# Kernel tuning notes

Hardware: AMD Instinct MI355X
Metric: run time of the kernel (lower is better)

## Reference

```python
import jax, jax.numpy as jnp
import numpy as np

B, D_IN, E, H, V = 4096, 4096, 2048, 2048, 32000


def setup_inputs() -> dict:
    key = jax.random.key(0)
    ks = jax.random.split(key, 24)
    s = 0.02
    p = lambda k, shape: (jax.random.normal(k, shape, dtype=jnp.float32) * s)
    return {
        "input": jax.random.normal(ks[0], (B, D_IN), dtype=jnp.float32),
        "hidden": jnp.zeros((B, H), dtype=jnp.float32),
        "cell": jnp.zeros((B, H), dtype=jnp.float32),
        # embedding linear (input_size -> emb_size), stored as [in, out]
        "We": p(ks[1], (D_IN, E)), "be": p(ks[2], (E,)),
        # x-to-gate linears (emb -> hidden)
        "Wf": p(ks[3], (E, H)), "bf": p(ks[4], (H,)),
        "Wi": p(ks[5], (E, H)), "bi": p(ks[6], (H,)),
        "Wc": p(ks[7], (E, H)), "bc": p(ks[8], (H,)),
        "Wo": p(ks[9], (E, H)), "bo": p(ks[10], (H,)),
        # hidden-to-gate linears (hidden -> hidden)
        "Uf": p(ks[11], (H, H)), "bhf": p(ks[12], (H,)),
        "Ui": p(ks[13], (H, H)), "bhi": p(ks[14], (H,)),
        "Uc": p(ks[15], (H, H)), "bhc": p(ks[16], (H,)),
        "Uo": p(ks[17], (H, H)), "bho": p(ks[18], (H,)),
        # output head (hidden -> output_size)
        "Wend": p(ks[19], (H, V)), "bend": p(ks[20], (V,)),
    }


def reference(input, hidden, cell,
              We, be, Wf, bf, Wi, bi, Wc, bc, Wo, bo,
              Uf, bhf, Ui, bhi, Uc, bhc, Uo, bho, Wend, bend):
    # embedded = Linear(input)
    emb = input @ We + be                                  # [B, E]
    f = jax.nn.sigmoid(emb @ Wf + bf + hidden @ Uf + bhf)  # forget gate [B, H]
    i = jax.nn.sigmoid(emb @ Wi + bi + hidden @ Ui + bhi)  # input gate
    g = jnp.tanh(emb @ Wc + bc + hidden @ Uc + bhc)        # candidate cell
    new_cell = f * cell + i * g
    o = jax.nn.sigmoid(emb @ Wo + bo + hidden @ Uo + bho)  # output gate
    new_hidden = o * jnp.tanh(new_cell)
    out = jax.nn.log_softmax(new_hidden @ Wend + bend, axis=1)  # [B, V]
    return (out, new_hidden, new_cell)
```

## Files before the change

kernel.cpp:

```cpp
#include <hip/hip_runtime.h>
#include <stdint.h>

#define B_DIM 4096
#define DIN   4096
#define E_DIM 2048
#define H_DIM 2048
#define V_DIM 32000

typedef __attribute__((ext_vector_type(8))) short s8v;
typedef __attribute__((ext_vector_type(4))) float f4v;
typedef __attribute__((ext_vector_type(4))) int   i4v;
typedef __attribute__((ext_vector_type(8))) int   i8v;
typedef __attribute__((ext_vector_type(4))) uint  u4v;
typedef __attribute__((ext_vector_type(4))) float f4n;

__device__ __forceinline__ ushort f2bf(float f) {
    union { float f; uint32_t u; } v; v.f = f;
    uint32_t u = v.u;
    return (ushort)((u + 0x7FFFu + ((u >> 16) & 1u)) >> 16);
}
__device__ __forceinline__ float bf2f(ushort h) {
    union { uint32_t u; float f; } v; v.u = ((uint32_t)h) << 16;
    return v.f;
}

__device__ __forceinline__ uint8_t f2fp8(float x) {
    union { float f; uint32_t u; } v; v.f = x;
    uint8_t sign = (uint8_t)((v.u >> 24) & 0x80u);
    uint32_t a = v.u & 0x7FFFFFFFu;
    if (a >= 0x43E00000u) return sign | 0x7E;
    uint32_t r = a + 0x0007FFFFu + ((a >> 20) & 1u);
    int e = (int)(r >> 23) - 127 + 7;
    if (e <= 0) {
        float s = fabsf(x);
        int q = (int)(s * 512.0f + 0.5f);
        if (q > 7) q = 7;
        return sign | (uint8_t)q;
    }
    uint32_t m = (r >> 20) & 7u;
    uint8_t b = (uint8_t)((e << 3) | m);
    if (b == 0x7F) b = 0x7E;
    return sign | b;
}

__global__ void k_cvt(const float* __restrict__ src, ushort* __restrict__ dst, int n4) {
    int i = blockIdx.x * blockDim.x + threadIdx.x;
    if (i >= n4) return;
    float4 v = *(const float4*)(src + (size_t)i * 4);
    ushort4 o;
    o.x = f2bf(v.x); o.y = f2bf(v.y); o.z = f2bf(v.z); o.w = f2bf(v.w);
    *(ushort4*)(dst + (size_t)i * 4) = o;
}

__global__ void k_cvt_hidden(const float* __restrict__ src, ushort* __restrict__ dst) {
    int i = blockIdx.x * blockDim.x + threadIdx.x;
    int b = i >> 9;
    int c = (i & 511) << 2;
    float4 v = *(const float4*)(src + (size_t)b * H_DIM + c);
    ushort4 o;
    o.x = f2bf(v.x); o.y = f2bf(v.y); o.z = f2bf(v.z); o.w = f2bf(v.w);
    *(ushort4*)(dst + (size_t)b * 4096 + 2048 + c) = o;
}

__global__ void k_transpose_bf16(const float* __restrict__ src, ushort* __restrict__ dst,
                                 int srcCols, int dstStride, int dstRowOff, int dstColOff) {
    __shared__ float tile[32][33];
    int tx = threadIdx.x, ty = threadIdx.y;
    int n0 = blockIdx.x * 32, k0 = blockIdx.y * 32;
#pragma unroll
    for (int i = 0; i < 4; i++)
        tile[ty + 8 * i][tx] = src[(size_t)(k0 + ty + 8 * i) * srcCols + n0 + tx];
    __syncthreads();
#pragma unroll
    for (int i = 0; i < 4; i++) {
        int n = ty + 8 * i;
        dst[(size_t)(dstRowOff + n0 + n) * dstStride + dstColOff + k0 + tx] = f2bf(tile[tx][n]);
    }
}

__global__ void k_transpose_fp8(const float* __restrict__ src, uint8_t* __restrict__ dst,
                                int srcCols, int dstStride) {
    __shared__ float tile[32][33];
    int tx = threadIdx.x, ty = threadIdx.y;
    int n0 = blockIdx.x * 32, k0 = blockIdx.y * 32;
#pragma unroll
    for (int i = 0; i < 4; i++)
        tile[ty + 8 * i][tx] = src[(size_t)(k0 + ty + 8 * i) * srcCols + n0 + tx];
    __syncthreads();
#pragma unroll
    for (int i = 0; i < 4; i++) {
        int n = ty + 8 * i;
        dst[(size_t)(n0 + n) * dstStride + k0 + tx] = f2fp8(tile[tx][n] * 32.0f);
    }
}

__global__ void k_transpose_gate8(const float* __restrict__ W0, const float* __restrict__ W1,
                                  const float* __restrict__ W2, const float* __restrict__ W3,
                                  const float* __restrict__ U0, const float* __restrict__ U1,
                                  const float* __restrict__ U2, const float* __restrict__ U3,
                                  ushort* __restrict__ dst) {
    const float* srcs[8] = {W0, W1, W2, W3, U0, U1, U2, U3};
    int z = blockIdx.z;
    const float* src = srcs[z];
    int g = z & 3;
    int dstColOff = (z >> 2) << 11;
    __shared__ float tile[32][33];
    int tx = threadIdx.x, ty = threadIdx.y;
    int n0 = blockIdx.x * 32, k0 = blockIdx.y * 32;
#pragma unroll
    for (int i = 0; i < 4; i++)
        tile[ty + 8 * i][tx] = src[(size_t)(k0 + ty + 8 * i) * H_DIM + n0 + tx];
    __syncthreads();
#pragma unroll
    for (int i = 0; i < 4; i++) {
        int h = n0 + ty + 8 * i;
        int drow = ((h >> 5) << 7) + (((h >> 4) & 1) << 6) + (g << 4) + (h & 15);
        dst[(size_t)drow * 4096 + dstColOff + k0 + tx] = f2bf(tile[tx][ty + 8 * i]);
    }
}

__global__ void k_biaspack(const float* __restrict__ b0, const float* __restrict__ bh0,
                           const float* __restrict__ b1, const float* __restrict__ bh1,
                           const float* __restrict__ b2, const float* __restrict__ bh2,
                           const float* __restrict__ b3, const float* __restrict__ bh3,
                           float* __restrict__ out) {
    int h = blockIdx.x * blockDim.x + threadIdx.x;
    if (h >= H_DIM) return;
    int base = ((h >> 5) << 7) + (((h >> 4) & 1) << 6) + (h & 15);
    out[base]      = b0[h] + bh0[h];
    out[base + 16] = b1[h] + bh1[h];
    out[base + 32] = b2[h] + bh2[h];
    out[base + 48] = b3[h] + bh3[h];
}

template<int EPI>
__global__ __launch_bounds__(256, 2)
void k_gemm_bt(const ushort* __restrict__ A, const ushort* __restrict__ Bt,
               void* __restrict__ Cv, const float* __restrict__ bias,
               int M, int N, int K, int lda, int ldb, int ldc,
               const float* __restrict__ cell, float* __restrict__ outH,
               float* __restrict__ outC, uint8_t* __restrict__ hidF8) {
    __shared__ __align__(16) ushort ldsA[128 * 64];
    __shared__ __align__(16) ushort ldsB[128 * 64];
    const int t = threadIdx.x;
    const int wid = t >> 6, lane = t & 63;

    int bid = blockIdx.x;
    int mt  = ((bid & 7) << 2) | ((bid >> 3) & 3);
    int nt  = bid >> 5;
    int m0  = mt << 7, n0 = nt << 7;

    f4v acc[4][4];
#pragma unroll
    for (int i = 0; i < 4; i++)
#pragma unroll
        for (int j = 0; j < 4; j++) acc[i][j] = (f4v){0.f, 0.f, 0.f, 0.f};

    const int wr = wid >> 1, wc = wid & 1;

    const int kTiles = K >> 6;
    for (int kt = 0; kt < kTiles; ++kt) {
#pragma unroll
        for (int c = 0; c < 4; ++c) {
            int idx = c * 256 + wid * 64 + lane;
            int row = idx >> 3;
            int kb  = (idx & 7) << 4;
            const ushort* gA = A  + (size_t)(m0 + row) * lda + (kt << 6) + (kb >> 1);
            const ushort* gB = Bt + (size_t)(n0 + row) * ldb + (kt << 6) + (kb >> 1);
            char* lA = (char*)ldsA + (size_t)(c * 256 + wid * 64) * 16;
            char* lB = (char*)ldsB + (size_t)(c * 256 + wid * 64) * 16;
            __builtin_amdgcn_global_load_lds((const __attribute__((address_space(1))) void*)gA,
                                             (__attribute__((address_space(3))) void*)lA, 16, 0, 0);
            __builtin_amdgcn_global_load_lds((const __attribute__((address_space(1))) void*)gB,
                                             (__attribute__((address_space(3))) void*)lB, 16, 0, 0);
        }
        __syncthreads();

#pragma unroll
        for (int ks = 0; ks < 2; ++ks) {
            s8v af[4], bfr[4];
#pragma unroll
            for (int m = 0; m < 4; ++m) {
                int r = wr * 64 + m * 16 + (lane & 15);
                int kb = ks * 64 + ((lane >> 4) << 4);
                af[m] = *(const s8v*)((const char*)ldsA + r * 128 + kb);
            }
#pragma unroll
            for (int n = 0; n < 4; ++n) {
                int r = wc * 64 + n * 16 + (lane & 15);
                int kb = ks * 64 + ((lane >> 4) << 4);
                bfr[n] = *(const s8v*)((const char*)ldsB + r * 128 + kb);
            }
#pragma unroll
            for (int m = 0; m < 4; ++m)
#pragma unroll
                for (int n = 0; n < 4; ++n)
                    acc[m][n] = __builtin_amdgcn_mfma_f32_16x16x32_bf16(af[m], bfr[n], acc[m][n], 0, 0, 0);
        }
        __syncthreads();
    }

    if (EPI == 1) {
#pragma unroll
        for (int n = 0; n < 4; ++n) {
            int cg = n0 + wc * 64 + n * 16 + (lane & 15);
            float bv = bias[cg];
#pragma unroll
            for (int m = 0; m < 4; ++m) {
                int rbase = m0 + wr * 64 + m * 16 + ((lane >> 4) << 2);
#pragma unroll
                for (int r = 0; r < 4; ++r)
                    ((ushort*)Cv)[(size_t)(rbase + r) * ldc + cg] = f2bf(acc[m][n][r] + bv);
            }
        }
    } else {
        int h = (n0 >> 2) + wc * 16 + (lane & 15);
        float bv[4];
#pragma unroll
        for (int n = 0; n < 4; ++n) bv[n] = bias[n0 + wc * 64 + n * 16 + (lane & 15)];
#pragma unroll
        for (int m = 0; m < 4; ++m) {
            int rbase = m0 + wr * 64 + m * 16 + ((lane >> 4) << 2);
#pragma unroll
            for (int r = 0; r < 4; ++r) {
                int b = rbase + r;
                float pf_ = acc[m][0][r] + bv[0];
                float pi_ = acc[m][1][r] + bv[1];
                float pc_ = acc[m][2][r] + bv[2];
                float po_ = acc[m][3][r] + bv[3];
                float fg = 1.f / (1.f + __expf(-pf_));
                float ig = 1.f / (1.f + __expf(-pi_));
                float gg = tanhf(pc_);
                float og = 1.f / (1.f + __expf(-po_));
                size_t off = (size_t)b * H_DIM + h;
                float nc = fg * cell[off] + ig * gg;
                float nh = og * tanhf(nc);
                outC[off] = nc;
                outH[off] = nh;
                hidF8[off] = f2fp8(nh * 8.0f);
            }
        }
    }
}

__global__ __launch_bounds__(256, 3)
void k_gemm_mx(const uint8_t* __restrict__ A, const uint8_t* __restrict__ Bt,
               ushort* __restrict__ Lbf, const float* __restrict__ bias,
               float2* __restrict__ partials, int N, int K, int ldc, int ncb) {
    __shared__ __align__(16) uint8_t ldsAB[2][128 * 128];
    __shared__ float2 smStat[256];
    const int t = threadIdx.x;
    const int wid = t >> 6, lane = t & 63;
    const int wrr = wid >> 1, wcc = wid & 1;

    int bid = blockIdx.x;
    int mt  = ((bid & 7) << 2) | ((bid >> 3) & 3);
    int nt  = bid >> 5;
    int m0  = mt << 7, n0 = nt << 7;

    int offA[4], offB[4];
#pragma unroll
    for (int c = 0; c < 4; ++c) {
        int idx = c * 256 + t;
        int row = idx >> 3;
        int cb  = ((idx & 7) ^ (row & 7)) << 4;
        offA[c] = (m0 + row) * K + cb;
        offB[c] = (n0 + row) * K + cb;
    }

    f4v acc[4][4];
#pragma unroll
    for (int i = 0; i < 4; ++i)
#pragma unroll
        for (int j = 0; j < 4; ++j) acc[i][j] = (f4v){0.f, 0.f, 0.f, 0.f};

    const int l15 = lane & 15;
    const int sw  = (lane & 7) << 4;
    const int o0  = ((lane >> 4) << 5) ^ sw;
    const int o1  = o0 ^ 16;

    const int kTiles = K >> 7;
    for (int kt = 0; kt < kTiles; ++kt) {
#pragma unroll
        for (int c = 0; c < 4; ++c) {
            __builtin_amdgcn_global_load_lds(
                (const __attribute__((address_space(1))) void*)(A + offA[c] + (kt << 7)),
                (__attribute__((address_space(3))) void*)&ldsAB[0][(c * 256 + wid * 64) * 16], 16, 0, 0);
            __builtin_amdgcn_global_load_lds(
                (const __attribute__((address_space(1))) void*)(Bt + offB[c] + (kt << 7)),
                (__attribute__((address_space(3))) void*)&ldsAB[1][(c * 256 + wid * 64) * 16], 16, 0, 0);
        }
        __syncthreads();

        i8v af[4], bf[4];
#pragma unroll
        for (int m = 0; m < 4; ++m) {
            int row = wrr * 64 + m * 16 + l15;
            i4v lo = *(const i4v*)&ldsAB[0][row * 128 + o0];
            i4v hi = *(const i4v*)&ldsAB[0][row * 128 + o1];
            af[m] = __builtin_shufflevector(lo, hi, 0, 1, 2, 3, 4, 5, 6, 7);
        }
#pragma unroll
        for (int n = 0; n < 4; ++n) {
            int row = wcc * 64 + n * 16 + l15;
            i4v lo = *(const i4v*)&ldsAB[1][row * 128 + o0];
            i4v hi = *(const i4v*)&ldsAB[1][row * 128 + o1];
            bf[n] = __builtin_shufflevector(lo, hi, 0, 1, 2, 3, 4, 5, 6, 7);
        }
#pragma unroll
        for (int m = 0; m < 4; ++m)
#pragma unroll
            for (int n = 0; n < 4; ++n)
                acc[m][n] = __builtin_amdgcn_mfma_scale_f32_16x16x128_f8f6f4(
                    af[m], bf[n], acc[m][n], 0, 0, 0, 124, 0, 122);
        __syncthreads();
    }

    float bv[4];
#pragma unroll
    for (int n = 0; n < 4; ++n) bv[n] = bias[n0 + wcc * 64 + n * 16 + l15];
    ushort* ctile = (ushort*)&ldsAB[0][0];
#pragma unroll
    for (int m = 0; m < 4; ++m) {
#pragma unroll
        for (int r = 0; r < 4; ++r) {
            int rl = wrr * 64 + m * 16 + ((lane >> 4) << 2) + r;
            float v[4];
#pragma unroll
            for (int n = 0; n < 4; ++n) {
                v[n] = acc[m][n][r] + bv[n];
                ctile[rl * 128 + wcc * 64 + n * 16 + l15] = f2bf(v[n]);
            }
            float mx = fmaxf(fmaxf(v[0], v[1]), fmaxf(v[2], v[3]));
            float ss = __expf(v[0] - mx) + __expf(v[1] - mx) +
                       __expf(v[2] - mx) + __expf(v[3] - mx);
#pragma unroll
            for (int off = 1; off < 16; off <<= 1) {
                float mo = __shfl_xor(mx, off);
                float so = __shfl_xor(ss, off);
                float nm = fmaxf(mx, mo);
                ss = ss * __expf(mx - nm) + so * __expf(mo - nm);
                mx = nm;
            }
            if (l15 == 0) smStat[wcc * 128 + rl] = make_float2(mx, ss);
        }
    }
    __syncthreads();
    if (t < 128) {
        float2 a = smStat[t], b = smStat[128 + t];
        float M = fmaxf(a.x, b.x);
        float S = a.y * __expf(a.x - M) + b.y * __expf(b.x - M);
        partials[(size_t)(m0 + t) * ncb + nt] = make_float2(M, S);
    }
#pragma unroll
    for (int i = 0; i < 8; ++i) {
        int idx = i * 256 + t;
        int row = idx >> 4;
        int c16 = idx & 15;
        u4v val = *(const u4v*)&ctile[row * 128 + c16 * 8];
        __builtin_nontemporal_store(val, (u4v*)&Lbf[(size_t)(m0 + row) * ldc + n0 + c16 * 8]);
    }
}

__global__ void k_lsefin(const float2* __restrict__ part, float* __restrict__ lse, int ncb) {
    int row = blockIdx.x;
    int l = threadIdx.x;
    float M = -1e30f, S = 0.f;
    for (int i = l; i < ncb; i += 64) {
        float2 p = part[(size_t)row * ncb + i];
        float nm = fmaxf(M, p.x);
        S = S * __expf(M - nm) + p.y * __expf(p.x - nm);
        M = nm;
    }
#pragma unroll
    for (int off = 1; off < 64; off <<= 1) {
        float Mo = __shfl_xor(M, off);
        float So = __shfl_xor(S, off);
        float nm = fmaxf(M, Mo);
        S = S * __expf(M - nm) + So * __expf(Mo - nm);
        M = nm;
    }
    if (l == 0) lse[row] = M + logf(S);
}

__global__ void k_norm(const ushort* __restrict__ Lbf, const float* __restrict__ lse,
                       float* __restrict__ out) {
    int b = blockIdx.y;
    int c8 = blockIdx.x * blockDim.x + threadIdx.x;
    if (c8 >= V_DIM / 8) return;
    float l = lse[b];
    const u4v* src = (const u4v*)(Lbf + (size_t)b * V_DIM + (size_t)c8 * 8);
    u4v pv = __builtin_nontemporal_load(src);
    f4n q0, q1;
    q0.x = bf2f((ushort)(pv.x & 0xFFFF)) - l;
    q0.y = bf2f((ushort)(pv.x >> 16)) - l;
    q0.z = bf2f((ushort)(pv.y & 0xFFFF)) - l;
    q0.w = bf2f((ushort)(pv.y >> 16)) - l;
    q1.x = bf2f((ushort)(pv.z & 0xFFFF)) - l;
    q1.y = bf2f((ushort)(pv.z >> 16)) - l;
    q1.z = bf2f((ushort)(pv.w & 0xFFFF)) - l;
    q1.w = bf2f((ushort)(pv.w >> 16)) - l;
    float* dst = out + (size_t)b * V_DIM + (size_t)c8 * 8;
    __builtin_nontemporal_store(q0, (f4n*)dst);
    __builtin_nontemporal_store(q1, (f4n*)(dst + 4));
}

extern "C" void kernel_launch(void* const* d_in, const int* in_sizes, int n_in,
                              void* d_out, int out_size, void* d_ws, size_t ws_size,
                              hipStream_t stream) {
    const float* in_input  = (const float*)d_in[0];
    const float* in_hidden = (const float*)d_in[1];
    const float* in_cell   = (const float*)d_in[2];
    const float* We   = (const float*)d_in[3];
    const float* be   = (const float*)d_in[4];
    const float* Wf   = (const float*)d_in[5];
    const float* bfv  = (const float*)d_in[6];
    const float* Wi   = (const float*)d_in[7];
    const float* biv  = (const float*)d_in[8];
    const float* Wc   = (const float*)d_in[9];
    const float* bcv  = (const float*)d_in[10];
    const float* Wo   = (const float*)d_in[11];
    const float* bov  = (const float*)d_in[12];
    const float* Uf   = (const float*)d_in[13];
    const float* bhf  = (const float*)d_in[14];
    const float* Ui   = (const float*)d_in[15];
    const float* bhi  = (const float*)d_in[16];
    const float* Uc   = (const float*)d_in[17];
    const float* bhc  = (const float*)d_in[18];
    const float* Uo   = (const float*)d_in[19];
    const float* bho  = (const float*)d_in[20];
    const float* Wend = (const float*)d_in[21];
    const float* bend = (const float*)d_in[22];

    char* ws = (char*)d_ws;
    const size_t oWendF8 = 0;
    const size_t oHidF8  = oWendF8 + (size_t)V_DIM * H_DIM;
    const size_t oBias2  = oHidF8 + (size_t)B_DIM * H_DIM;
    const size_t oLse    = oBias2 + 4 * H_DIM * 4;
    const size_t oPart   = oLse + B_DIM * 4;
    const size_t oR      = oPart + (size_t)B_DIM * 250 * 8;
    const size_t oAin    = oR;
    const size_t oWeT    = oAin + (size_t)B_DIM * DIN * 2;
    const size_t oA2     = oWeT + (size_t)E_DIM * DIN * 2;
    const size_t oWUT    = oA2  + (size_t)B_DIM * 4096 * 2;

    uint8_t* WendF8 = (uint8_t*)(ws + oWendF8);
    uint8_t* hidF8  = (uint8_t*)(ws + oHidF8);
    float*   bias2  = (float*)(ws + oBias2);
    float*   lse    = (float*)(ws + oLse);
    float2*  part   = (float2*)(ws + oPart);
    ushort*  Lbf    = (ushort*)(ws + oR);
    ushort*  Ain    = (ushort*)(ws + oAin);
    ushort*  WeT    = (ushort*)(ws + oWeT);
    ushort*  A2     = (ushort*)(ws + oA2);
    ushort*  WUT    = (ushort*)(ws + oWUT);

    float* out  = (float*)d_out;
    float* outH = out + (size_t)B_DIM * V_DIM;
    float* outC = outH + (size_t)B_DIM * H_DIM;

    const int NCB = V_DIM / 128;

    dim3 blk256(256), blk64(64);

    k_cvt<<<dim3((B_DIM * DIN / 4) / 256), blk256, 0, stream>>>(in_input, Ain, B_DIM * DIN / 4);
    k_cvt_hidden<<<dim3((B_DIM * H_DIM / 4) / 256), blk256, 0, stream>>>(in_hidden, A2);

    dim3 tb(32, 8);
    k_transpose_bf16<<<dim3(E_DIM / 32, DIN / 32), tb, 0, stream>>>(We, WeT, E_DIM, DIN, 0, 0);
    k_transpose_gate8<<<dim3(H_DIM / 32, E_DIM / 32, 8), tb, 0, stream>>>(
        Wf, Wi, Wc, Wo, Uf, Ui, Uc, Uo, WUT);
    k_transpose_fp8<<<dim3(V_DIM / 32, H_DIM / 32), tb, 0, stream>>>(Wend, WendF8, V_DIM, H_DIM);
    k_biaspack<<<dim3(H_DIM / 256), blk256, 0, stream>>>(bfv, bhf, biv, bhi, bcv, bhc, bov, bho, bias2);

    k_gemm_bt<1><<<dim3((B_DIM / 128) * (E_DIM / 128)), blk256, 0, stream>>>(
        Ain, WeT, A2, be, B_DIM, E_DIM, DIN, DIN, DIN, 4096,
        nullptr, nullptr, nullptr, nullptr);

    k_gemm_bt<2><<<dim3((B_DIM / 128) * (8192 / 128)), blk256, 0, stream>>>(
        A2, WUT, nullptr, bias2, B_DIM, 8192, 4096, 4096, 4096, 0,
        in_cell, outH, outC, hidF8);

    k_gemm_mx<<<dim3((B_DIM / 128) * (V_DIM / 128)), blk256, 0, stream>>>(
        hidF8, WendF8, Lbf, bend, part, V_DIM, H_DIM, V_DIM, NCB);

    k_lsefin<<<dim3(B_DIM), blk64, 0, stream>>>(part, lse, NCB);
    k_norm<<<dim3(16, B_DIM), blk256, 0, stream>>>(Lbf, lse, out);
}
```

Baseline: 1.193 ms.

## Run fused gate GEMM in FP8 with scaled MFMA instead of BF16

Converts the embedding output, hidden state and packed gate weights to FP8 with a 32x scale, and replaces the BF16 gate GEMM with a new FP8 kernel using the scaled 16x16x128 MFMA and direct global-to-LDS loads with swizzling. The LSTM epilogue moves into the new kernel, and the embedding GEMM now writes FP8 directly. This is meant to double matrix throughput and halve operand traffic for the largest GEMM before the output head. It lowers accuracy of the gate pre-activations.

```diff
diff --git a/kernel.cpp b/kernel.cpp
--- a/kernel.cpp
+++ b/kernel.cpp
@@ -52,14 +52,15 @@
     *(ushort4*)(dst + (size_t)i * 4) = o;
 }
 
-__global__ void k_cvt_hidden(const float* __restrict__ src, ushort* __restrict__ dst) {
+__global__ void k_cvt_hidden(const float* __restrict__ src, uint8_t* __restrict__ dst) {
     int i = blockIdx.x * blockDim.x + threadIdx.x;
     int b = i >> 9;
     int c = (i & 511) << 2;
     float4 v = *(const float4*)(src + (size_t)b * H_DIM + c);
-    ushort4 o;
-    o.x = f2bf(v.x); o.y = f2bf(v.y); o.z = f2bf(v.z); o.w = f2bf(v.w);
-    *(ushort4*)(dst + (size_t)b * 4096 + 2048 + c) = o;
+    uchar4 o;
+    o.x = f2fp8(v.x * 32.0f); o.y = f2fp8(v.y * 32.0f);
+    o.z = f2fp8(v.z * 32.0f); o.w = f2fp8(v.w * 32.0f);
+    *(uchar4*)(dst + (size_t)b * 4096 + 2048 + c) = o;
 }
 
 __global__ void k_transpose_bf16(const float* __restrict__ src, ushort* __restrict__ dst,
@@ -98,7 +99,7 @@
                                   const float* __restrict__ W2, const float* __restrict__ W3,
                                   const float* __restrict__ U0, const float* __restrict__ U1,
                                   const float* __restrict__ U2, const float* __restrict__ U3,
-                                  ushort* __restrict__ dst) {
+                                  uint8_t* __restrict__ dst) {
     const float* srcs[8] = {W0, W1, W2, W3, U0, U1, U2, U3};
     int z = blockIdx.z;
     const float* src = srcs[z];
@@ -115,7 +116,7 @@
     for (int i = 0; i < 4; i++) {
         int h = n0 + ty + 8 * i;
         int drow = ((h >> 5) << 7) + (((h >> 4) & 1) << 6) + (g << 4) + (h & 15);
-        dst[(size_t)drow * 4096 + dstColOff + k0 + tx] = f2bf(tile[tx][ty + 8 * i]);
+        dst[(size_t)drow * 4096 + dstColOff + k0 + tx] = f2fp8(tile[tx][ty + 8 * i] * 32.0f);
     }
 }
 
@@ -133,13 +134,10 @@
     out[base + 48] = b3[h] + bh3[h];
 }
 
-template<int EPI>
 __global__ __launch_bounds__(256, 2)
 void k_gemm_bt(const ushort* __restrict__ A, const ushort* __restrict__ Bt,
-               void* __restrict__ Cv, const float* __restrict__ bias,
-               int M, int N, int K, int lda, int ldb, int ldc,
-               const float* __restrict__ cell, float* __restrict__ outH,
-               float* __restrict__ outC, uint8_t* __restrict__ hidF8) {
+               uint8_t* __restrict__ Cf8, const float* __restrict__ bias,
+               int N, int K, int lda, int ldb, int ldc) {
     __shared__ __align__(16) ushort ldsA[128 * 64];
     __shared__ __align__(16) ushort ldsB[128 * 64];
     const int t = threadIdx.x;
@@ -200,45 +198,117 @@
         __syncthreads();
     }
 
-    if (EPI == 1) {
-#pragma unroll
-        for (int n = 0; n < 4; ++n) {
-            int cg = n0 + wc * 64 + n * 16 + (lane & 15);
-            float bv = bias[cg];
-#pragma unroll
-            for (int m = 0; m < 4; ++m) {
-                int rbase = m0 + wr * 64 + m * 16 + ((lane >> 4) << 2);
-#pragma unroll
-                for (int r = 0; r < 4; ++r)
-                    ((ushort*)Cv)[(size_t)(rbase + r) * ldc + cg] = f2bf(acc[m][n][r] + bv);
-            }
-        }
-    } else {
-        int h = (n0 >> 2) + wc * 16 + (lane & 15);
-        float bv[4];
-#pragma unroll
-        for (int n = 0; n < 4; ++n) bv[n] = bias[n0 + wc * 64 + n * 16 + (lane & 15)];
+#pragma unroll
+    for (int n = 0; n < 4; ++n) {
+        int cg = n0 + wc * 64 + n * 16 + (lane & 15);
+        float bv = bias[cg];
 #pragma unroll
         for (int m = 0; m < 4; ++m) {
             int rbase = m0 + wr * 64 + m * 16 + ((lane >> 4) << 2);
 #pragma unroll
-            for (int r = 0; r < 4; ++r) {
-                int b = rbase + r;
-                float pf_ = acc[m][0][r] + bv[0];
-                float pi_ = acc[m][1][r] + bv[1];
-                float pc_ = acc[m][2][r] + bv[2];
-                float po_ = acc[m][3][r] + bv[3];
-                float fg = 1.f / (1.f + __expf(-pf_));
-                float ig = 1.f / (1.f + __expf(-pi_));
-                float gg = tanhf(pc_);
-                float og = 1.f / (1.f + __expf(-po_));
-                size_t off = (size_t)b * H_DIM + h;
-                float nc = fg * cell[off] + ig * gg;
-                float nh = og * tanhf(nc);
-                outC[off] = nc;
-                outH[off] = nh;
-                hidF8[off] = f2fp8(nh * 8.0f);
-            }
+            for (int r = 0; r < 4; ++r)
+                Cf8[(size_t)(rbase + r) * ldc + cg] = f2fp8((acc[m][n][r] + bv) * 32.0f);
+        }
+    }
+}
+
+__global__ __launch_bounds__(256, 3)
+void k_gatemx(const uint8_t* __restrict__ A, const uint8_t* __restrict__ Bt,
+              const float* __restrict__ bias, const float* __restrict__ cell,
+              float* __restrict__ outH, float* __restrict__ outC,
+              uint8_t* __restrict__ hidF8) {
+    __shared__ __align__(16) uint8_t ldsAB[2][128 * 128];
+    const int t = threadIdx.x;
+    const int wid = t >> 6, lane = t & 63;
+    const int wrr = wid >> 1, wcc = wid & 1;
+
+    int bid = blockIdx.x;
+    int mt  = ((bid & 7) << 2) | ((bid >> 3) & 3);
+    int nt  = bid >> 5;
+    int m0  = mt << 7, n0 = nt << 7;
+    const int K = 4096;
+
+    int offA[4], offB[4];
+#pragma unroll
+    for (int c = 0; c < 4; ++c) {
+        int idx = c * 256 + t;
+        int row = idx >> 3;
+        int cb  = ((idx & 7) ^ (row & 7)) << 4;
+        offA[c] = (m0 + row) * K + cb;
+        offB[c] = (n0 + row) * K + cb;
+    }
+
+    f4v acc[4][4];
+#pragma unroll
+    for (int i = 0; i < 4; ++i)
+#pragma unroll
+        for (int j = 0; j < 4; ++j) acc[i][j] = (f4v){0.f, 0.f, 0.f, 0.f};
+
+    const int l15 = lane & 15;
+    const int sw  = (lane & 7) << 4;
+    const int o0  = ((lane >> 4) << 5) ^ sw;
+    const int o1  = o0 ^ 16;
+
+    const int kTiles = K >> 7;
+    for (int kt = 0; kt < kTiles; ++kt) {
+#pragma unroll
+        for (int c = 0; c < 4; ++c) {
+            __builtin_amdgcn_global_load_lds(
+                (const __attribute__((address_space(1))) void*)(A + offA[c] + (kt << 7)),
+                (__attribute__((address_space(3))) void*)&ldsAB[0][(c * 256 + wid * 64) * 16], 16, 0, 0);
+            __builtin_amdgcn_global_load_lds(
+                (const __attribute__((address_space(1))) void*)(Bt + offB[c] + (kt << 7)),
+                (__attribute__((address_space(3))) void*)&ldsAB[1][(c * 256 + wid * 64) * 16], 16, 0, 0);
+        }
+        __syncthreads();
+
+        i8v af[4], bf[4];
+#pragma unroll
+        for (int m = 0; m < 4; ++m) {
+            int row = wrr * 64 + m * 16 + l15;
+            i4v lo = *(const i4v*)&ldsAB[0][row * 128 + o0];
+            i4v hi = *(const i4v*)&ldsAB[0][row * 128 + o1];
+            af[m] = __builtin_shufflevector(lo, hi, 0, 1, 2, 3, 4, 5, 6, 7);
+        }
+#pragma unroll
+        for (int n = 0; n < 4; ++n) {
+            int row = wcc * 64 + n * 16 + l15;
+            i4v lo = *(const i4v*)&ldsAB[1][row * 128 + o0];
+            i4v hi = *(const i4v*)&ldsAB[1][row * 128 + o1];
+            bf[n] = __builtin_shufflevector(lo, hi, 0, 1, 2, 3, 4, 5, 6, 7);
+        }
+#pragma unroll
+        for (int m = 0; m < 4; ++m)
+#pragma unroll
+            for (int n = 0; n < 4; ++n)
+                acc[m][n] = __builtin_amdgcn_mfma_scale_f32_16x16x128_f8f6f4(
+                    af[m], bf[n], acc[m][n], 0, 0, 0, 122, 0, 122);
+        __syncthreads();
+    }
+
+    int h = (n0 >> 2) + wcc * 16 + l15;
+    float bv[4];
+#pragma unroll
+    for (int n = 0; n < 4; ++n) bv[n] = bias[n0 + wcc * 64 + n * 16 + l15];
+#pragma unroll
+    for (int m = 0; m < 4; ++m) {
+#pragma unroll
+        for (int r = 0; r < 4; ++r) {
+            int b = m0 + wrr * 64 + m * 16 + ((lane >> 4) << 2) + r;
+            float pf_ = acc[m][0][r] + bv[0];
+            float pi_ = acc[m][1][r] + bv[1];
+            float pc_ = acc[m][2][r] + bv[2];
+            float po_ = acc[m][3][r] + bv[3];
+            float fg = 1.f / (1.f + __expf(-pf_));
+            float ig = 1.f / (1.f + __expf(-pi_));
+            float gg = tanhf(pc_);
+            float og = 1.f / (1.f + __expf(-po_));
+            size_t off = (size_t)b * H_DIM + h;
+            float nc = fg * cell[off] + ig * gg;
+            float nh = og * tanhf(nc);
+            outC[off] = nc;
+            outH[off] = nh;
+            hidF8[off] = f2fp8(nh * 8.0f);
         }
     }
 }
@@ -442,7 +512,7 @@
     const size_t oAin    = oR;
     const size_t oWeT    = oAin + (size_t)B_DIM * DIN * 2;
     const size_t oA2     = oWeT + (size_t)E_DIM * DIN * 2;
-    const size_t oWUT    = oA2  + (size_t)B_DIM * 4096 * 2;
+    const size_t oWUT8   = oA2  + (size_t)B_DIM * 4096;
 
     uint8_t* WendF8 = (uint8_t*)(ws + oWendF8);
     uint8_t* hidF8  = (uint8_t*)(ws + oHidF8);
@@ -452,8 +522,8 @@
     ushort*  Lbf    = (ushort*)(ws + oR);
     ushort*  Ain    = (ushort*)(ws + oAin);
     ushort*  WeT    = (ushort*)(ws + oWeT);
-    ushort*  A2     = (ushort*)(ws + oA2);
-    ushort*  WUT    = (ushort*)(ws + oWUT);
+    uint8_t* A2     = (uint8_t*)(ws + oA2);
+    uint8_t* WUT8   = (uint8_t*)(ws + oWUT8);
 
     float* out  = (float*)d_out;
     float* outH = out + (size_t)B_DIM * V_DIM;
@@ -469,17 +539,15 @@
     dim3 tb(32, 8);
     k_transpose_bf16<<<dim3(E_DIM / 32, DIN / 32), tb, 0, stream>>>(We, WeT, E_DIM, DIN, 0, 0);
     k_transpose_gate8<<<dim3(H_DIM / 32, E_DIM / 32, 8), tb, 0, stream>>>(
-        Wf, Wi, Wc, Wo, Uf, Ui, Uc, Uo, WUT);
+        Wf, Wi, Wc, Wo, Uf, Ui, Uc, Uo, WUT8);
     k_transpose_fp8<<<dim3(V_DIM / 32, H_DIM / 32), tb, 0, stream>>>(Wend, WendF8, V_DIM, H_DIM);
     k_biaspack<<<dim3(H_DIM / 256), blk256, 0, stream>>>(bfv, bhf, biv, bhi, bcv, bhc, bov, bho, bias2);
 
-    k_gemm_bt<1><<<dim3((B_DIM / 128) * (E_DIM / 128)), blk256, 0, stream>>>(
-        Ain, WeT, A2, be, B_DIM, E_DIM, DIN, DIN, DIN, 4096,
-        nullptr, nullptr, nullptr, nullptr);
-
-    k_gemm_bt<2><<<dim3((B_DIM / 128) * (8192 / 128)), blk256, 0, stream>>>(
-        A2, WUT, nullptr, bias2, B_DIM, 8192, 4096, 4096, 4096, 0,
-        in_cell, outH, outC, hidF8);
+    k_gemm_bt<<<dim3((B_DIM / 128) * (E_DIM / 128)), blk256, 0, stream>>>(
+        Ain, WeT, A2, be, E_DIM, DIN, DIN, DIN, 4096);
+
+    k_gatemx<<<dim3((B_DIM / 128) * (8192 / 128)), blk256, 0, stream>>>(
+        A2, WUT8, bias2, in_cell, outH, outC, hidF8);
 
     k_gemm_mx<<<dim3((B_DIM / 128) * (V_DIM / 128)), blk256, 0, stream>>>(
         hidF8, WendF8, Lbf, bend, part, V_DIM, H_DIM, V_DIM, NCB);
```

After: 1.020 ms. 14.5% less time.
